# Optimization experiments

Measured on AMD Instinct MI355X. Metric: run time of the kernel, lower is better.

Reference implementation:

```python
import jax, jax.numpy as jnp
import numpy as np

NUM_HEADS = 16
BLOCK_SIZE = 512


def setup_inputs() -> dict:
    key = jax.random.key(0)
    ks = jax.random.split(key, 5)
    B, S, D = 2, 4096, 1024
    scale = 1.0 / np.sqrt(D)
    return {
        "x": jax.random.normal(ks[0], (B, S, D), dtype=jnp.float32),
        "w_q": jax.random.normal(ks[1], (D, D), dtype=jnp.float32) * scale,
        "w_k": jax.random.normal(ks[2], (D, D), dtype=jnp.float32) * scale,
        "w_v": jax.random.normal(ks[3], (D, D), dtype=jnp.float32) * scale,
        "w_o": jax.random.normal(ks[4], (D, D), dtype=jnp.float32) * scale,
    }


def _ring_attention(q, k, v, block_size):
    # q,k,v: [B, H, S, Dh]; online-softmax accumulation over KV blocks
    B, H, S, Dh = q.shape
    scale = 1.0 / np.sqrt(Dh).astype(np.float32)
    nb = S // block_size
    # [nb, B, H, block, Dh] so lax.scan iterates over KV blocks
    kb = k.reshape(B, H, nb, block_size, Dh).transpose(2, 0, 1, 3, 4)
    vb = v.reshape(B, H, nb, block_size, Dh).transpose(2, 0, 1, 3, 4)

    m0 = jnp.full((B, H, S), -jnp.inf, dtype=q.dtype)
    l0 = jnp.zeros((B, H, S), dtype=q.dtype)
    o0 = jnp.zeros((B, H, S, Dh), dtype=q.dtype)

    def step(carry, kv):
        m, l, o = carry
        kj, vj = kv                                   # [B,H,block,Dh]
        s = jnp.einsum("bhqd,bhkd->bhqk", q, kj) * scale  # [B,H,S,block]
        m_new = jnp.maximum(m, s.max(axis=-1))
        alpha = jnp.exp(m - m_new)                    # rescale old stats
        p = jnp.exp(s - m_new[..., None])             # unnormalized probs
        o = o * alpha[..., None] + jnp.einsum("bhqk,bhkd->bhqd", p, vj)
        l = l * alpha + p.sum(axis=-1)
        return (m_new, l, o), None

    (m, l, o), _ = jax.lax.scan(step, (m0, l0, o0), (kb, vb))
    return o / l[..., None]


def reference(x, w_q, w_k, w_v, w_o):
    B, S, D = x.shape
    H = NUM_HEADS
    Dh = D // H
    q = (x @ w_q).reshape(B, S, H, Dh).transpose(0, 2, 1, 3)
    k = (x @ w_k).reshape(B, S, H, Dh).transpose(0, 2, 1, 3)
    v = (x @ w_v).reshape(B, S, H, Dh).transpose(0, 2, 1, 3)
    out = _ring_attention(q, k, v, BLOCK_SIZE)        # [B,H,S,Dh]
    out = out.transpose(0, 2, 1, 3).reshape(B, S, D)
    return out @ w_o
```

## Files before the change

### kernel.cpp

```cpp
#include <hip/hip_runtime.h>
#include <stdint.h>

#define B_ 2
#define S_ 4096
#define D_ 1024
#define H_ 16
#define DH_ 64
#define M_ 8192

typedef __attribute__((ext_vector_type(8))) short short8;
typedef __attribute__((ext_vector_type(4))) float f32x4;
typedef __attribute__((ext_vector_type(16))) float f32x16;
typedef __attribute__((ext_vector_type(2))) unsigned int uint2v;
typedef __attribute__((ext_vector_type(4))) unsigned int uint4v;

__device__ __forceinline__ unsigned short f2bf(float f) {
  union { float f; unsigned int u; } v; v.f = f;
  return (unsigned short)((v.u + 0x7FFFu + ((v.u >> 16) & 1u)) >> 16);
}

__device__ __forceinline__ unsigned int cvtpk_bf16(float lo, float hi) {
  unsigned int r;
  asm("v_cvt_pk_bf16_f32 %0, %1, %2" : "=v"(r) : "v"(lo), "v"(hi));
  return r;
}

__device__ __forceinline__ void gld_lds16(const void* g, void* l) {
  __builtin_amdgcn_global_load_lds(
      (const __attribute__((address_space(1))) void*)g,
      (__attribute__((address_space(3))) void*)l, 16, 0, 0);
}

__global__ void conv_x(const float* __restrict__ X, unsigned short* __restrict__ Xb) {
  size_t i = ((size_t)blockIdx.x * 256 + threadIdx.x) * 8;
  float4 a = *(const float4*)(X + i);
  float4 b = *(const float4*)(X + i + 4);
  uint4 pk;
  pk.x = (unsigned int)f2bf(a.x) | ((unsigned int)f2bf(a.y) << 16);
  pk.y = (unsigned int)f2bf(a.z) | ((unsigned int)f2bf(a.w) << 16);
  pk.z = (unsigned int)f2bf(b.x) | ((unsigned int)f2bf(b.y) << 16);
  pk.w = (unsigned int)f2bf(b.z) | ((unsigned int)f2bf(b.w) << 16);
  *(uint4*)(Xb + i) = pk;
}

__global__ void conv_w(const float* __restrict__ W0, const float* __restrict__ W1,
                       const float* __restrict__ W2, const float* __restrict__ W3,
                       unsigned short* __restrict__ T0, unsigned short* __restrict__ T1,
                       unsigned short* __restrict__ T2, unsigned short* __restrict__ T3) {
  int z = blockIdx.y;
  const float* W = (z == 0) ? W0 : (z == 1) ? W1 : (z == 2) ? W2 : W3;
  unsigned short* T = (z == 0) ? T0 : (z == 1) ? T1 : (z == 2) ? T2 : T3;
  int o = blockIdx.x * 256 + threadIdx.x;
  int nn = o >> 7;
  int k0 = (o & 127) * 8;
  unsigned short t[8];
  #pragma unroll
  for (int i = 0; i < 8; ++i) t[i] = f2bf(W[(size_t)(k0 + i) * D_ + nn]);
  uint4 pk;
  pk.x = (unsigned int)t[0] | ((unsigned int)t[1] << 16);
  pk.y = (unsigned int)t[2] | ((unsigned int)t[3] << 16);
  pk.z = (unsigned int)t[4] | ((unsigned int)t[5] << 16);
  pk.w = (unsigned int)t[6] | ((unsigned int)t[7] << 16);
  *(uint4*)(T + (size_t)nn * D_ + k0) = pk;
}

__global__ __launch_bounds__(256, 2)
void gemm_qkv(const unsigned short* __restrict__ Xb,
              const unsigned short* __restrict__ Wq,
              const unsigned short* __restrict__ Wk,
              const unsigned short* __restrict__ Wv,
              unsigned short* __restrict__ Qb,
              unsigned short* __restrict__ Kb,
              unsigned short* __restrict__ Vtb) {
  __shared__ char As[16384];
  __shared__ char Bs[16384];
  const int tid = threadIdx.x, wave = tid >> 6, lane = tid & 63;
  const int lg = lane >> 4, ll = lane & 15;
  const int m0 = blockIdx.x * 128, n0 = blockIdx.y * 128, z = blockIdx.z;
  const unsigned short* Wt = (z == 0) ? Wq : ((z == 1) ? Wk : Wv);
  const int wr = wave >> 1, wc = wave & 1;
  f32x4 acc[4][4];
  #pragma unroll
  for (int a = 0; a < 4; ++a)
    #pragma unroll
    for (int b = 0; b < 4; ++b) acc[a][b] = (f32x4){0.f, 0.f, 0.f, 0.f};

  const char* Ag = (const char*)Xb;
  const char* Bg = (const char*)Wt;
  for (int kt = 0; kt < 16; ++kt) {
    __syncthreads();
    #pragma unroll
    for (int i = 0; i < 2; ++i) {
      int s0 = wave * 256 + i * 128 + lane;
      int row0 = s0 >> 3, colb0 = (s0 & 7) * 16;
      gld_lds16(Ag + (size_t)(m0 + row0) * 2048 + kt * 128 + colb0, As + wave * 4096 + i * 2048);
      gld_lds16(Bg + (size_t)(n0 + row0) * 2048 + kt * 128 + colb0, Bs + wave * 4096 + i * 2048);
      int s1 = s0 + 64;
      int row1 = s1 >> 3, colb1 = (s1 & 7) * 16;
      gld_lds16(Ag + (size_t)(m0 + row1) * 2048 + kt * 128 + colb1, As + wave * 4096 + i * 2048 + 1024);
      gld_lds16(Bg + (size_t)(n0 + row1) * 2048 + kt * 128 + colb1, Bs + wave * 4096 + i * 2048 + 1024);
    }
    __syncthreads();
    #pragma unroll
    for (int c = 0; c < 2; ++c) {
      short8 af[4], bf[4];
      #pragma unroll
      for (int i = 0; i < 4; ++i) {
        af[i] = *(const short8*)(As + (wr * 64 + i * 16 + ll) * 128 + lg * 16 + c * 64);
        bf[i] = *(const short8*)(Bs + (wc * 64 + i * 16 + ll) * 128 + lg * 16 + c * 64);
      }
      #pragma unroll
      for (int mi = 0; mi < 4; ++mi)
        #pragma unroll
        for (int ni = 0; ni < 4; ++ni)
          acc[mi][ni] = __builtin_amdgcn_mfma_f32_16x16x32_bf16(af[mi], bf[ni], acc[mi][ni], 0, 0, 0);
    }
  }

  if (z < 2) {
    unsigned short* Out = (z == 0) ? Qb : Kb;
    const float sc = (z == 0) ? 0.18033688011112042f : 1.0f;
    #pragma unroll
    for (int mi = 0; mi < 4; ++mi)
      #pragma unroll
      for (int ni = 0; ni < 4; ++ni)
        #pragma unroll
        for (int j = 0; j < 4; ++j) {
          int m = m0 + wr * 64 + mi * 16 + lg * 4 + j;
          int n = n0 + wc * 64 + ni * 16 + ll;
          int bh = (m >> 12) * H_ + (n >> 6);
          Out[((size_t)bh * S_ + (m & 4095)) * DH_ + (n & 63)] = f2bf(acc[mi][ni][j] * sc);
        }
  } else {
    #pragma unroll
    for (int mi = 0; mi < 4; ++mi)
      #pragma unroll
      for (int ni = 0; ni < 4; ++ni) {
        int mb = m0 + wr * 64 + mi * 16 + lg * 4;
        int n = n0 + wc * 64 + ni * 16 + ll;
        int bh = (mb >> 12) * H_ + (n >> 6);
        uint2 pk;
        pk.x = (unsigned int)f2bf(acc[mi][ni][0]) | ((unsigned int)f2bf(acc[mi][ni][1]) << 16);
        pk.y = (unsigned int)f2bf(acc[mi][ni][2]) | ((unsigned int)f2bf(acc[mi][ni][3]) << 16);
        *(uint2*)(Vtb + ((size_t)bh * DH_ + (n & 63)) * S_ + (mb & 4095)) = pk;
      }
  }
}

__global__ __launch_bounds__(128, 2)
void attn_kernel(const unsigned short* __restrict__ Qb,
                 const unsigned short* __restrict__ Kb,
                 const unsigned short* __restrict__ Vtb,
                 unsigned short* __restrict__ Ob) {
  __shared__ char lds[24576];
  const int tid = threadIdx.x;
  const int wave = tid >> 6, lane = tid & 63;
  const int hh = lane >> 5;
  const int ql = lane & 31;

  const int hw = blockIdx.x;
  const int virt = (hw & 7) * 128 + (hw >> 3);
  const int bh = virt >> 5, qblk = virt & 31;
  const int qbase = qblk * 128 + wave * 64;

  const char* Qg = (const char*)Qb + (size_t)bh * S_ * 128;
  short8 qa[4], qb2[4];
  #pragma unroll
  for (int c = 0; c < 4; ++c) {
    qa[c]  = *(const short8*)(Qg + (size_t)(qbase + ql) * 128 + c * 32 + hh * 16);
    qb2[c] = *(const short8*)(Qg + (size_t)(qbase + 32 + ql) * 128 + c * 32 + hh * 16);
  }

  f32x16 oa0, oa1, ob0, ob1, mC;
  #pragma unroll
  for (int i = 0; i < 16; ++i) { oa0[i] = 0.f; oa1[i] = 0.f; ob0[i] = 0.f; ob1[i] = 0.f; mC[i] = -12.0f; }
  float la = 0.f, lb = 0.f;

  const char* Kg = (const char*)Kb + (size_t)bh * S_ * 128;
  const char* Vg = (const char*)Vtb + (size_t)bh * (size_t)DH_ * S_ * 2;

  const int koff = (lane >> 3) * 128 + (((lane & 7) ^ (lane >> 3)) << 4);
  const size_t voff = (size_t)(lane >> 2) * 8192 + ((((lane & 3) ^ ((lane >> 3) & 3))) << 4);

#define STAGE(off, t) do { \
    if (wave == 0) { \
      const char* kp = Kg + (size_t)(t) * 4096 + koff; \
      gld_lds16(kp,        lds + (off)); \
      gld_lds16(kp + 1024, lds + (off) + 1024); \
      gld_lds16(kp + 2048, lds + (off) + 2048); \
      gld_lds16(kp + 3072, lds + (off) + 3072); \
    } else { \
      const char* vp = Vg + (size_t)(t) * 64 + voff; \
      gld_lds16(vp,            lds + 12288 + (off)); \
      gld_lds16(vp + 131072,   lds + 12288 + (off) + 1024); \
      gld_lds16(vp + 262144,   lds + 12288 + (off) + 2048); \
      gld_lds16(vp + 393216,   lds + 12288 + (off) + 3072); \
    } \
  } while (0)

#define COMPUTE(off) do { \
    f32x16 pa, pb; \
    __builtin_amdgcn_s_setprio(1); \
    { \
      short8 kf = *(const short8*)(lds + (off) + ((ql * 128 + hh * 16) ^ ((ql & 7) << 4))); \
      pa = __builtin_amdgcn_mfma_f32_32x32x16_bf16(kf, qa[0], mC, 0, 0, 0); \
      pb = __builtin_amdgcn_mfma_f32_32x32x16_bf16(kf, qb2[0], mC, 0, 0, 0); \
    } \
    _Pragma("unroll") \
    for (int c = 1; c < 4; ++c) { \
      short8 kf = *(const short8*)(lds + (off) + ((ql * 128 + c * 32 + hh * 16) ^ ((ql & 7) << 4))); \
      pa = __builtin_amdgcn_mfma_f32_32x32x16_bf16(kf, qa[c], pa, 0, 0, 0); \
      pb = __builtin_amdgcn_mfma_f32_32x32x16_bf16(kf, qb2[c], pb, 0, 0, 0); \
    } \
    __builtin_amdgcn_s_setprio(0); \
    _Pragma("unroll") \
    for (int i = 0; i < 16; ++i) pa[i] = __builtin_amdgcn_exp2f(pa[i]); \
    uint4v pqa0, pqa1; \
    { \
      uint2v r; \
      r = __builtin_amdgcn_permlane32_swap(cvtpk_bf16(pa[0], pa[1]), cvtpk_bf16(pa[4], pa[5]), false, false); \
      pqa0.x = r[0]; pqa0.z = r[1]; \
      r = __builtin_amdgcn_permlane32_swap(cvtpk_bf16(pa[2], pa[3]), cvtpk_bf16(pa[6], pa[7]), false, false); \
      pqa0.y = r[0]; pqa0.w = r[1]; \
      r = __builtin_amdgcn_permlane32_swap(cvtpk_bf16(pa[8], pa[9]), cvtpk_bf16(pa[12], pa[13]), false, false); \
      pqa1.x = r[0]; pqa1.z = r[1]; \
      r = __builtin_amdgcn_permlane32_swap(cvtpk_bf16(pa[10], pa[11]), cvtpk_bf16(pa[14], pa[15]), false, false); \
      pqa1.y = r[0]; pqa1.w = r[1]; \
    } \
    _Pragma("unroll") \
    for (int i = 0; i < 16; ++i) pb[i] = __builtin_amdgcn_exp2f(pb[i]); \
    uint4v pqb0, pqb1; \
    { \
      uint2v r; \
      r = __builtin_amdgcn_permlane32_swap(cvtpk_bf16(pb[0], pb[1]), cvtpk_bf16(pb[4], pb[5]), false, false); \
      pqb0.x = r[0]; pqb0.z = r[1]; \
      r = __builtin_amdgcn_permlane32_swap(cvtpk_bf16(pb[2], pb[3]), cvtpk_bf16(pb[6], pb[7]), false, false); \
      pqb0.y = r[0]; pqb0.w = r[1]; \
      r = __builtin_amdgcn_permlane32_swap(cvtpk_bf16(pb[8], pb[9]), cvtpk_bf16(pb[12], pb[13]), false, false); \
      pqb1.x = r[0]; pqb1.z = r[1]; \
      r = __builtin_amdgcn_permlane32_swap(cvtpk_bf16(pb[10], pb[11]), cvtpk_bf16(pb[14], pb[15]), false, false); \
      pqb1.y = r[0]; pqb1.w = r[1]; \
    } \
    __builtin_amdgcn_s_setprio(1); \
    { \
      short8 vf0 = *(const short8*)(lds + 12288 + (off) + ((ql * 64 + hh * 16) ^ (((ql >> 1) & 3) << 4))); \
      short8 vf1 = *(const short8*)(lds + 12288 + (off) + (((32 + ql) * 64 + hh * 16) ^ (((ql >> 1) & 3) << 4))); \
      short8 psa = __builtin_bit_cast(short8, pqa0); \
      short8 psb = __builtin_bit_cast(short8, pqb0); \
      oa0 = __builtin_amdgcn_mfma_f32_32x32x16_bf16(vf0, psa, oa0, 0, 0, 0); \
      oa1 = __builtin_amdgcn_mfma_f32_32x32x16_bf16(vf1, psa, oa1, 0, 0, 0); \
      ob0 = __builtin_amdgcn_mfma_f32_32x32x16_bf16(vf0, psb, ob0, 0, 0, 0); \
      ob1 = __builtin_amdgcn_mfma_f32_32x32x16_bf16(vf1, psb, ob1, 0, 0, 0); \
    } \
    { \
      short8 vf0 = *(const short8*)(lds + 12288 + (off) + ((ql * 64 + 32 + hh * 16) ^ (((ql >> 1) & 3) << 4))); \
      short8 vf1 = *(const short8*)(lds + 12288 + (off) + (((32 + ql) * 64 + 32 + hh * 16) ^ (((ql >> 1) & 3) << 4))); \
      short8 psa = __builtin_bit_cast(short8, pqa1); \
      short8 psb = __builtin_bit_cast(short8, pqb1); \
      oa0 = __builtin_amdgcn_mfma_f32_32x32x16_bf16(vf0, psa, oa0, 0, 0, 0); \
      oa1 = __builtin_amdgcn_mfma_f32_32x32x16_bf16(vf1, psa, oa1, 0, 0, 0); \
      ob0 = __builtin_amdgcn_mfma_f32_32x32x16_bf16(vf0, psb, ob0, 0, 0, 0); \
      ob1 = __builtin_amdgcn_mfma_f32_32x32x16_bf16(vf1, psb, ob1, 0, 0, 0); \
    } \
    __builtin_amdgcn_s_setprio(0); \
    float sa0 = ((pa[0] + pa[1]) + (pa[2] + pa[3])) + ((pa[4] + pa[5]) + (pa[6] + pa[7])); \
    float sa1 = ((pa[8] + pa[9]) + (pa[10] + pa[11])) + ((pa[12] + pa[13]) + (pa[14] + pa[15])); \
    float sb0 = ((pb[0] + pb[1]) + (pb[2] + pb[3])) + ((pb[4] + pb[5]) + (pb[6] + pb[7])); \
    float sb1 = ((pb[8] + pb[9]) + (pb[10] + pb[11])) + ((pb[12] + pb[13]) + (pb[14] + pb[15])); \
    float ra = sa0 + sa1, rb = sb0 + sb1; \
    ra += __shfl_xor(ra, 32); \
    rb += __shfl_xor(rb, 32); \
    la += ra; lb += rb; \
  } while (0)

  STAGE(0, 0);
  STAGE(4096, 1);

  int oc = 0, on = 4096, os = 8192;
  for (int t = 0; t < 126; ++t) {
    asm volatile("s_waitcnt vmcnt(4)" ::: "memory");
    __builtin_amdgcn_s_barrier();
    STAGE(os, t + 2);
    __builtin_amdgcn_sched_barrier(0);
    COMPUTE(oc);
    int tmp = oc; oc = on; on = os; os = tmp;
  }
  asm volatile("s_waitcnt vmcnt(4)" ::: "memory");
  __builtin_amdgcn_s_barrier();
  __builtin_amdgcn_sched_barrier(0);
  COMPUTE(oc);
  { int tmp = oc; oc = on; on = os; os = tmp; }
  asm volatile("s_waitcnt vmcnt(0)" ::: "memory");
  __builtin_amdgcn_s_barrier();
  __builtin_amdgcn_sched_barrier(0);
  COMPUTE(oc);

  float inva = 1.f / la, invb = 1.f / lb;
  unsigned short* OpA = Ob + ((size_t)(bh >> 4) * S_ + qbase + ql) * D_ + (bh & 15) * DH_;
  unsigned short* OpB = Ob + ((size_t)(bh >> 4) * S_ + qbase + 32 + ql) * D_ + (bh & 15) * DH_;
  #pragma unroll
  for (int g = 0; g < 4; ++g) {
    uint2 pk2;
    pk2.x = (unsigned int)f2bf(oa0[4 * g + 0] * inva) | ((unsigned int)f2bf(oa0[4 * g + 1] * inva) << 16);
    pk2.y = (unsigned int)f2bf(oa0[4 * g + 2] * inva) | ((unsigned int)f2bf(oa0[4 * g + 3] * inva) << 16);
    *(uint2*)(OpA + g * 8 + hh * 4) = pk2;
    pk2.x = (unsigned int)f2bf(oa1[4 * g + 0] * inva) | ((unsigned int)f2bf(oa1[4 * g + 1] * inva) << 16);
    pk2.y = (unsigned int)f2bf(oa1[4 * g + 2] * inva) | ((unsigned int)f2bf(oa1[4 * g + 3] * inva) << 16);
    *(uint2*)(OpA + 32 + g * 8 + hh * 4) = pk2;
    pk2.x = (unsigned int)f2bf(ob0[4 * g + 0] * invb) | ((unsigned int)f2bf(ob0[4 * g + 1] * invb) << 16);
    pk2.y = (unsigned int)f2bf(ob0[4 * g + 2] * invb) | ((unsigned int)f2bf(ob0[4 * g + 3] * invb) << 16);
    *(uint2*)(OpB + g * 8 + hh * 4) = pk2;
    pk2.x = (unsigned int)f2bf(ob1[4 * g + 0] * invb) | ((unsigned int)f2bf(ob1[4 * g + 1] * invb) << 16);
    pk2.y = (unsigned int)f2bf(ob1[4 * g + 2] * invb) | ((unsigned int)f2bf(ob1[4 * g + 3] * invb) << 16);
    *(uint2*)(OpB + 32 + g * 8 + hh * 4) = pk2;
  }
#undef STAGE
#undef COMPUTE
}

__global__ __launch_bounds__(256, 2)
void gemm_o(const unsigned short* __restrict__ Ab,
            const unsigned short* __restrict__ Wo,
            float* __restrict__ Out) {
  __shared__ char As[16384];
  __shared__ char Bs[16384];
  const int tid = threadIdx.x, wave = tid >> 6, lane = tid & 63;
  const int lg = lane >> 4, ll = lane & 15;
  const int m0 = blockIdx.x * 128, n0 = blockIdx.y * 128;
  const int wr = wave >> 1, wc = wave & 1;
  f32x4 acc[4][4];
  #pragma unroll
  for (int a = 0; a < 4; ++a)
    #pragma unroll
    for (int b = 0; b < 4; ++b) acc[a][b] = (f32x4){0.f, 0.f, 0.f, 0.f};

  const char* Ag = (const char*)Ab;
  const char* Bg = (const char*)Wo;
  for (int kt = 0; kt < 16; ++kt) {
    __syncthreads();
    #pragma unroll
    for (int i = 0; i < 4; ++i) {
      int s = wave * 256 + i * 64 + lane;
      int row = s >> 3, colb = (s & 7) * 16;
      gld_lds16(Ag + (size_t)(m0 + row) * 2048 + kt * 128 + colb, As + wave * 4096 + i * 1024);
      gld_lds16(Bg + (size_t)(n0 + row) * 2048 + kt * 128 + colb, Bs + wave * 4096 + i * 1024);
    }
    __syncthreads();
    #pragma unroll
    for (int c = 0; c < 2; ++c) {
      short8 af[4], bf[4];
      #pragma unroll
      for (int i = 0; i < 4; ++i) {
        af[i] = *(const short8*)(As + (wr * 64 + i * 16 + ll) * 128 + lg * 16 + c * 64);
        bf[i] = *(const short8*)(Bs + (wc * 64 + i * 16 + ll) * 128 + lg * 16 + c * 64);
      }
      #pragma unroll
      for (int mi = 0; mi < 4; ++mi)
        #pragma unroll
        for (int ni = 0; ni < 4; ++ni)
          acc[mi][ni] = __builtin_amdgcn_mfma_f32_16x16x32_bf16(af[mi], bf[ni], acc[mi][ni], 0, 0, 0);
    }
  }
  #pragma unroll
  for (int mi = 0; mi < 4; ++mi)
    #pragma unroll
    for (int ni = 0; ni < 4; ++ni)
      #pragma unroll
      for (int j = 0; j < 4; ++j) {
        int m = m0 + wr * 64 + mi * 16 + lg * 4 + j;
        int n = n0 + wc * 64 + ni * 16 + ll;
        Out[(size_t)m * D_ + n] = acc[mi][ni][j];
      }
}

extern "C" void kernel_launch(void* const* d_in, const int* in_sizes, int n_in,
                              void* d_out, int out_size, void* d_ws, size_t ws_size,
                              hipStream_t stream) {
  const float* x  = (const float*)d_in[0];
  const float* wq = (const float*)d_in[1];
  const float* wk = (const float*)d_in[2];
  const float* wv = (const float*)d_in[3];
  const float* wo = (const float*)d_in[4];
  float* out = (float*)d_out;
  char* ws = (char*)d_ws;

  unsigned short* Xb = (unsigned short*)(ws);
  unsigned short* Wq = (unsigned short*)(ws + (16u << 20));
  unsigned short* Wk = (unsigned short*)(ws + (18u << 20));
  unsigned short* Wv = (unsigned short*)(ws + (20u << 20));
  unsigned short* Wo = (unsigned short*)(ws + (22u << 20));
  unsigned short* Qb = (unsigned short*)(ws + (24u << 20));
  unsigned short* Kb = (unsigned short*)(ws + (40u << 20));
  unsigned short* Vt = (unsigned short*)(ws + (56u << 20));
  unsigned short* Ob = (unsigned short*)(ws + (72u << 20));

  conv_x<<<dim3(4096), dim3(256), 0, stream>>>(x, Xb);
  conv_w<<<dim3(512, 4), dim3(256), 0, stream>>>(wq, wk, wv, wo, Wq, Wk, Wv, Wo);
  gemm_qkv<<<dim3(64, 8, 3), dim3(256), 0, stream>>>(Xb, Wq, Wk, Wv, Qb, Kb, Vt);
  attn_kernel<<<dim3(1024), dim3(128), 0, stream>>>(Qb, Kb, Vt, Ob);
  gemm_o<<<dim3(64, 8), dim3(256), 0, stream>>>(Ob, Wo, out);
}
```

Baseline: 282.7 us.

## Use single-wave attention workgroups with double-buffered self-staged K/V, no barriers

The attention kernel drops from two waves per workgroup (one loading K, one loading V, shared through a triple-buffered LDS ring with barriers) to one wave per workgroup that stages both K and V itself into a double buffer. The grid doubles to 2048 blocks and LDS per block shrinks. All K/V fragments for a tile are read into registers before the next tile is issued into the same buffer, so no workgroup barrier is needed. The aim is to remove barrier synchronisation and raise occupancy. The cost is a shallower prefetch and each wave doing twice the global-load work.

```diff
diff --git a/kernel.cpp b/kernel.cpp
--- a/kernel.cpp
+++ b/kernel.cpp
@@ -147,21 +147,20 @@
   }
 }
 
-__global__ __launch_bounds__(128, 2)
+__global__ __launch_bounds__(64, 2)
 void attn_kernel(const unsigned short* __restrict__ Qb,
                  const unsigned short* __restrict__ Kb,
                  const unsigned short* __restrict__ Vtb,
                  unsigned short* __restrict__ Ob) {
-  __shared__ char lds[24576];
-  const int tid = threadIdx.x;
-  const int wave = tid >> 6, lane = tid & 63;
+  __shared__ char lds[16384];
+  const int lane = threadIdx.x & 63;
   const int hh = lane >> 5;
   const int ql = lane & 31;
 
   const int hw = blockIdx.x;
-  const int virt = (hw & 7) * 128 + (hw >> 3);
-  const int bh = virt >> 5, qblk = virt & 31;
-  const int qbase = qblk * 128 + wave * 64;
+  const int virt = (hw & 7) * 256 + (hw >> 3);
+  const int bh = virt >> 6, qblk = virt & 63;
+  const int qbase = qblk * 64;
 
   const char* Qg = (const char*)Qb + (size_t)bh * S_ * 128;
   short8 qa[4], qb2[4];
@@ -170,6 +169,9 @@
     qa[c]  = *(const short8*)(Qg + (size_t)(qbase + ql) * 128 + c * 32 + hh * 16);
     qb2[c] = *(const short8*)(Qg + (size_t)(qbase + 32 + ql) * 128 + c * 32 + hh * 16);
   }
+  asm volatile("" : "+v"(qa[0]), "+v"(qa[1]), "+v"(qa[2]), "+v"(qa[3]),
+                    "+v"(qb2[0]), "+v"(qb2[1]), "+v"(qb2[2]), "+v"(qb2[3]));
+  asm volatile("s_waitcnt vmcnt(0)" ::: "memory");
 
   f32x16 oa0, oa1, ob0, ob1, mC;
   #pragma unroll
@@ -182,36 +184,51 @@
   const int koff = (lane >> 3) * 128 + (((lane & 7) ^ (lane >> 3)) << 4);
   const size_t voff = (size_t)(lane >> 2) * 8192 + ((((lane & 3) ^ ((lane >> 3) & 3))) << 4);
 
-#define STAGE(off, t) do { \
-    if (wave == 0) { \
-      const char* kp = Kg + (size_t)(t) * 4096 + koff; \
-      gld_lds16(kp,        lds + (off)); \
-      gld_lds16(kp + 1024, lds + (off) + 1024); \
-      gld_lds16(kp + 2048, lds + (off) + 2048); \
-      gld_lds16(kp + 3072, lds + (off) + 3072); \
-    } else { \
-      const char* vp = Vg + (size_t)(t) * 64 + voff; \
-      gld_lds16(vp,            lds + 12288 + (off)); \
-      gld_lds16(vp + 131072,   lds + 12288 + (off) + 1024); \
-      gld_lds16(vp + 262144,   lds + 12288 + (off) + 2048); \
-      gld_lds16(vp + 393216,   lds + 12288 + (off) + 3072); \
-    } \
+  const int kb = ql * 128;
+  const int kx0 = ((0 * 2 + hh) ^ (ql & 7)) << 4;
+  const int kx1 = ((1 * 2 + hh) ^ (ql & 7)) << 4;
+  const int kx2 = ((2 * 2 + hh) ^ (ql & 7)) << 4;
+  const int kx3 = ((3 * 2 + hh) ^ (ql & 7)) << 4;
+  const int vb0 = ql * 64, vb1 = (32 + ql) * 64;
+  const int vx0 = ((0 * 2 + hh) ^ ((ql >> 1) & 3)) << 4;
+  const int vx1 = ((1 * 2 + hh) ^ ((ql >> 1) & 3)) << 4;
+
+#define STAGE(KO, VO, t) do { \
+    const char* kp = Kg + (size_t)(t) * 4096 + koff; \
+    gld_lds16(kp,        lds + (KO)); \
+    gld_lds16(kp + 1024, lds + (KO) + 1024); \
+    gld_lds16(kp + 2048, lds + (KO) + 2048); \
+    gld_lds16(kp + 3072, lds + (KO) + 3072); \
+    const char* vp = Vg + (size_t)(t) * 64 + voff; \
+    gld_lds16(vp,          lds + (VO)); \
+    gld_lds16(vp + 131072, lds + (VO) + 1024); \
+    gld_lds16(vp + 262144, lds + (VO) + 2048); \
+    gld_lds16(vp + 393216, lds + (VO) + 3072); \
   } while (0)
 
-#define COMPUTE(off) do { \
+#define ITER(KO, VO, VMC, DOSTAGE, TN) do { \
+    asm volatile("s_waitcnt vmcnt(" #VMC ")" ::: "memory"); \
+    short8 kf0 = *(const short8*)(lds + (KO) + kb + kx0); \
+    short8 kf1 = *(const short8*)(lds + (KO) + kb + kx1); \
+    short8 kf2 = *(const short8*)(lds + (KO) + kb + kx2); \
+    short8 kf3 = *(const short8*)(lds + (KO) + kb + kx3); \
+    short8 vf00 = *(const short8*)(lds + (VO) + vb0 + vx0); \
+    short8 vf10 = *(const short8*)(lds + (VO) + vb1 + vx0); \
+    short8 vf01 = *(const short8*)(lds + (VO) + vb0 + vx1); \
+    short8 vf11 = *(const short8*)(lds + (VO) + vb1 + vx1); \
+    asm volatile("s_waitcnt lgkmcnt(0)" ::: "memory"); \
+    if (DOSTAGE) { STAGE(KO, VO, TN); } \
+    __builtin_amdgcn_sched_barrier(0); \
     f32x16 pa, pb; \
     __builtin_amdgcn_s_setprio(1); \
-    { \
-      short8 kf = *(const short8*)(lds + (off) + ((ql * 128 + hh * 16) ^ ((ql & 7) << 4))); \
-      pa = __builtin_amdgcn_mfma_f32_32x32x16_bf16(kf, qa[0], mC, 0, 0, 0); \
-      pb = __builtin_amdgcn_mfma_f32_32x32x16_bf16(kf, qb2[0], mC, 0, 0, 0); \
-    } \
-    _Pragma("unroll") \
-    for (int c = 1; c < 4; ++c) { \
-      short8 kf = *(const short8*)(lds + (off) + ((ql * 128 + c * 32 + hh * 16) ^ ((ql & 7) << 4))); \
-      pa = __builtin_amdgcn_mfma_f32_32x32x16_bf16(kf, qa[c], pa, 0, 0, 0); \
-      pb = __builtin_amdgcn_mfma_f32_32x32x16_bf16(kf, qb2[c], pb, 0, 0, 0); \
-    } \
+    pa = __builtin_amdgcn_mfma_f32_32x32x16_bf16(kf0, qa[0], mC, 0, 0, 0); \
+    pb = __builtin_amdgcn_mfma_f32_32x32x16_bf16(kf0, qb2[0], mC, 0, 0, 0); \
+    pa = __builtin_amdgcn_mfma_f32_32x32x16_bf16(kf1, qa[1], pa, 0, 0, 0); \
+    pb = __builtin_amdgcn_mfma_f32_32x32x16_bf16(kf1, qb2[1], pb, 0, 0, 0); \
+    pa = __builtin_amdgcn_mfma_f32_32x32x16_bf16(kf2, qa[2], pa, 0, 0, 0); \
+    pb = __builtin_amdgcn_mfma_f32_32x32x16_bf16(kf2, qb2[2], pb, 0, 0, 0); \
+    pa = __builtin_amdgcn_mfma_f32_32x32x16_bf16(kf3, qa[3], pa, 0, 0, 0); \
+    pb = __builtin_amdgcn_mfma_f32_32x32x16_bf16(kf3, qb2[3], pb, 0, 0, 0); \
     __builtin_amdgcn_s_setprio(0); \
     _Pragma("unroll") \
     for (int i = 0; i < 16; ++i) pa[i] = __builtin_amdgcn_exp2f(pa[i]); \
@@ -243,24 +260,20 @@
     } \
     __builtin_amdgcn_s_setprio(1); \
     { \
-      short8 vf0 = *(const short8*)(lds + 12288 + (off) + ((ql * 64 + hh * 16) ^ (((ql >> 1) & 3) << 4))); \
-      short8 vf1 = *(const short8*)(lds + 12288 + (off) + (((32 + ql) * 64 + hh * 16) ^ (((ql >> 1) & 3) << 4))); \
       short8 psa = __builtin_bit_cast(short8, pqa0); \
       short8 psb = __builtin_bit_cast(short8, pqb0); \
-      oa0 = __builtin_amdgcn_mfma_f32_32x32x16_bf16(vf0, psa, oa0, 0, 0, 0); \
-      oa1 = __builtin_amdgcn_mfma_f32_32x32x16_bf16(vf1, psa, oa1, 0, 0, 0); \
-      ob0 = __builtin_amdgcn_mfma_f32_32x32x16_bf16(vf0, psb, ob0, 0, 0, 0); \
-      ob1 = __builtin_amdgcn_mfma_f32_32x32x16_bf16(vf1, psb, ob1, 0, 0, 0); \
+      oa0 = __builtin_amdgcn_mfma_f32_32x32x16_bf16(vf00, psa, oa0, 0, 0, 0); \
+      oa1 = __builtin_amdgcn_mfma_f32_32x32x16_bf16(vf10, psa, oa1, 0, 0, 0); \
+      ob0 = __builtin_amdgcn_mfma_f32_32x32x16_bf16(vf00, psb, ob0, 0, 0, 0); \
+      ob1 = __builtin_amdgcn_mfma_f32_32x32x16_bf16(vf10, psb, ob1, 0, 0, 0); \
     } \
     { \
-      short8 vf0 = *(const short8*)(lds + 12288 + (off) + ((ql * 64 + 32 + hh * 16) ^ (((ql >> 1) & 3) << 4))); \
-      short8 vf1 = *(const short8*)(lds + 12288 + (off) + (((32 + ql) * 64 + 32 + hh * 16) ^ (((ql >> 1) & 3) << 4))); \
       short8 psa = __builtin_bit_cast(short8, pqa1); \
       short8 psb = __builtin_bit_cast(short8, pqb1); \
-      oa0 = __builtin_amdgcn_mfma_f32_32x32x16_bf16(vf0, psa, oa0, 0, 0, 0); \
-      oa1 = __builtin_amdgcn_mfma_f32_32x32x16_bf16(vf1, psa, oa1, 0, 0, 0); \
-      ob0 = __builtin_amdgcn_mfma_f32_32x32x16_bf16(vf0, psb, ob0, 0, 0, 0); \
-      ob1 = __builtin_amdgcn_mfma_f32_32x32x16_bf16(vf1, psb, ob1, 0, 0, 0); \
+      oa0 = __builtin_amdgcn_mfma_f32_32x32x16_bf16(vf01, psa, oa0, 0, 0, 0); \
+      oa1 = __builtin_amdgcn_mfma_f32_32x32x16_bf16(vf11, psa, oa1, 0, 0, 0); \
+      ob0 = __builtin_amdgcn_mfma_f32_32x32x16_bf16(vf01, psb, ob0, 0, 0, 0); \
+      ob1 = __builtin_amdgcn_mfma_f32_32x32x16_bf16(vf11, psb, ob1, 0, 0, 0); \
     } \
     __builtin_amdgcn_s_setprio(0); \
     float sa0 = ((pa[0] + pa[1]) + (pa[2] + pa[3])) + ((pa[4] + pa[5]) + (pa[6] + pa[7])); \
@@ -273,27 +286,15 @@
     la += ra; lb += rb; \
   } while (0)
 
-  STAGE(0, 0);
-  STAGE(4096, 1);
-
-  int oc = 0, on = 4096, os = 8192;
-  for (int t = 0; t < 126; ++t) {
-    asm volatile("s_waitcnt vmcnt(4)" ::: "memory");
-    __builtin_amdgcn_s_barrier();
-    STAGE(os, t + 2);
-    __builtin_amdgcn_sched_barrier(0);
-    COMPUTE(oc);
-    int tmp = oc; oc = on; on = os; os = tmp;
-  }
-  asm volatile("s_waitcnt vmcnt(4)" ::: "memory");
-  __builtin_amdgcn_s_barrier();
-  __builtin_amdgcn_sched_barrier(0);
-  COMPUTE(oc);
-  { int tmp = oc; oc = on; on = os; os = tmp; }
-  asm volatile("s_waitcnt vmcnt(0)" ::: "memory");
-  __builtin_amdgcn_s_barrier();
-  __builtin_amdgcn_sched_barrier(0);
-  COMPUTE(oc);
+  STAGE(0, 8192, 0);
+  STAGE(4096, 12288, 1);
+
+  for (int t = 0; t < 126; t += 2) {
+    ITER(0, 8192, 8, 1, t + 2);
+    ITER(4096, 12288, 8, 1, t + 3);
+  }
+  ITER(0, 8192, 8, 0, 0);
+  ITER(4096, 12288, 0, 0, 0);
 
   float inva = 1.f / la, invb = 1.f / lb;
   unsigned short* OpA = Ob + ((size_t)(bh >> 4) * S_ + qbase + ql) * D_ + (bh & 15) * DH_;
@@ -315,7 +316,7 @@
     *(uint2*)(OpB + 32 + g * 8 + hh * 4) = pk2;
   }
 #undef STAGE
-#undef COMPUTE
+#undef ITER
 }
 
 __global__ __launch_bounds__(256, 2)
@@ -397,6 +398,6 @@
   conv_x<<<dim3(4096), dim3(256), 0, stream>>>(x, Xb);
   conv_w<<<dim3(512, 4), dim3(256), 0, stream>>>(wq, wk, wv, wo, Wq, Wk, Wv, Wo);
   gemm_qkv<<<dim3(64, 8, 3), dim3(256), 0, stream>>>(Xb, Wq, Wk, Wv, Qb, Kb, Vt);
-  attn_kernel<<<dim3(1024), dim3(128), 0, stream>>>(Qb, Kb, Vt, Ob);
+  attn_kernel<<<dim3(2048), dim3(64), 0, stream>>>(Qb, Kb, Vt, Ob);
   gemm_o<<<dim3(64, 8), dim3(256), 0, stream>>>(Ob, Wo, out);
 }
```

Result: slower. 302.3 us (+6.9%).
